# Performance work log

Measured on AMD Instinct MI355X. Metric: run time of the kernel, lower is better.

The kernel has to match this reference:

```python
import jax, jax.numpy as jnp
import numpy as np

C = 128  # num_hidden[-1]; nheads = 1 so dim == C
L, H, W = 16, 96, 96


def conv5(x, w):
    # x: [N, Cin, H, W], w: [1, Cin, 5, 5]; padding=2 -> SAME
    return jax.lax.conv_general_dilated(
        x, w, window_strides=(1, 1), padding=[(2, 2), (2, 2)],
        dimension_numbers=('NCHW', 'OIHW', 'NCHW'))


def setup_inputs() -> dict:
    key = jax.random.key(0)
    ks = jax.random.split(key, 9)
    s = 0.05
    return dict(
        x=jax.random.normal(ks[0], (L, C, H, W), jnp.float32),
        Wq=jax.random.normal(ks[1], (C, C), jnp.float32) * s,
        bq=jax.random.normal(ks[2], (C,), jnp.float32) * s,
        Wk=jax.random.normal(ks[3], (C, C), jnp.float32) * s,
        bk=jax.random.normal(ks[4], (C,), jnp.float32) * s,
        Wv=jax.random.normal(ks[5], (C, C), jnp.float32) * s,
        bv=jax.random.normal(ks[6], (C,), jnp.float32) * s,
        Wa=jax.random.normal(ks[7], (1, 2 * C, 5, 5), jnp.float32) * s,
        ba=jax.random.normal(ks[8], (1,), jnp.float32) * s,
    )


def reference(x, Wq, bq, Wk, bk, Wv, bv, Wa, ba):
    # 1x1 convs == per-pixel linear maps
    Q = jnp.einsum('lchw,dc->ldhw', x, Wq) + bq[None, :, None, None]
    K = jnp.einsum('lchw,dc->ldhw', x, Wk) + bk[None, :, None, None]
    V = jnp.einsum('lchw,dc->ldhw', x, Wv) + bv[None, :, None, None]
    # conv5x5(cat(Qi, Kj)) = conv5x5(Qi; Wa_q) + conv5x5(Kj; Wa_k) + ba
    Aq = conv5(Q, Wa[:, :C])[:, 0]   # [L, H, W]
    Ak = conv5(K, Wa[:, C:])[:, 0]   # [L, H, W]
    S = Aq[:, None] + Ak[None, :] + ba[0]       # [L, L, H, W] score maps H_ij
    A = jax.nn.softmax(S, axis=1)               # softmax over key frame j
    out = jnp.einsum('ijhw,jchw->ichw', A, V)   # weighted sum of V over j
    return out
```

## Files before the change

kernel.cpp:

```cpp
#include <hip/hip_runtime.h>


#define HW    9216
#define HDIM  96
#define WDIM  96
#define CDIM  128
#define WP    28
#define WGS   904

__device__ __forceinline__ void fma4(float4& a, const float4& x, const float4& s) {
    a.x += x.x * s.x; a.y += x.y * s.y; a.z += x.z * s.z; a.w += x.w * s.w;
}
__device__ __forceinline__ void axpy4(float4& o, float w, const float4& v) {
    o.x += w * v.x; o.y += w * v.y; o.z += w * v.z; o.w += w * v.w;
}

__global__ void k_prep(const float* __restrict__ Wk, const float* __restrict__ Wa,
                       const float* __restrict__ Wv,
                       float* __restrict__ weffp, float* __restrict__ wvt) {
    const int b = blockIdx.x;
    if (b < 14) {
        int idx = b * 256 + threadIdx.x;
        if (idx < 128 * WP) {
            int cp = idx / WP, tap = idx % WP;
            float s = 0.f;
            if (tap < 25)
                for (int c = 0; c < 128; ++c)
                    s += Wk[c * 128 + cp] * Wa[(128 + c) * 25 + tap];
            weffp[idx] = s;
        }
    } else {
        int idx = (b - 14) * 256 + threadIdx.x;
        wvt[(idx & 127) * 128 + (idx >> 7)] = Wv[idx];
    }
}

__global__ __launch_bounds__(256, 2) void k_z(const float* __restrict__ x,
                                              const float* __restrict__ weffp,
                                              float* __restrict__ z) {
    __shared__ float wsm[4 * WGS];
    const int tid = threadIdx.x;
    for (int i = tid; i < 4 * WGS; i += 256) {
        int cg = i / WGS, r = i % WGS;
        wsm[i] = (r < 896) ? weffp[cg * 896 + r] : 0.f;
    }
    __syncthreads();

    const int j    = blockIdx.y;
    const int w    = tid >> 6;
    const int lane = tid & 63;
    const int cg   = lane >> 4;
    const int lq   = lane & 15;
    const int px   = blockIdx.x * 256 + w * 64 + lq * 4;

    const float* xb = x + (size_t)(j * CDIM + cg * 32) * HW + px;
    const float* wg = wsm + cg * WGS;

    float4 acc[25];
    #pragma unroll
    for (int t = 0; t < 25; ++t) acc[t] = make_float4(0.f, 0.f, 0.f, 0.f);

    #pragma unroll 2
    for (int c = 0; c < 32; ++c) {
        float4 xv = *(const float4*)(xb + (size_t)c * HW);
        const float* wr = wg + c * WP;
        #pragma unroll
        for (int t = 0; t < 25; ++t) {
            float wv = wr[t];
            acc[t].x = fmaf(wv, xv.x, acc[t].x);
            acc[t].y = fmaf(wv, xv.y, acc[t].y);
            acc[t].z = fmaf(wv, xv.z, acc[t].z);
            acc[t].w = fmaf(wv, xv.w, acc[t].w);
        }
    }
    #pragma unroll
    for (int t = 0; t < 25; ++t) {
        acc[t].x += __shfl_xor(acc[t].x, 16, 64);
        acc[t].y += __shfl_xor(acc[t].y, 16, 64);
        acc[t].z += __shfl_xor(acc[t].z, 16, 64);
        acc[t].w += __shfl_xor(acc[t].w, 16, 64);
        acc[t].x += __shfl_xor(acc[t].x, 32, 64);
        acc[t].y += __shfl_xor(acc[t].y, 32, 64);
        acc[t].z += __shfl_xor(acc[t].z, 32, 64);
        acc[t].w += __shfl_xor(acc[t].w, 32, 64);
    }
    if (cg == 0) {
        float* zb = z + (size_t)j * 25 * HW + px;
        #pragma unroll
        for (int t = 0; t < 25; ++t)
            *(float4*)(zb + (size_t)t * HW) = acc[t];
    }
}

__global__ __launch_bounds__(256) void k_ak(const float* __restrict__ z,
                                            float* __restrict__ ak) {
    const int j  = blockIdx.y;
    const int px = blockIdx.x * 256 + threadIdx.x;
    const int h = px / WDIM, w = px % WDIM;
    const float* zb = z + (size_t)j * 25 * HW + px;
    float s = 0.f;
    #pragma unroll
    for (int kh = 0; kh < 5; ++kh) {
        const bool rok = (unsigned)(h + kh - 2) < (unsigned)HDIM;
        #pragma unroll
        for (int kw = 0; kw < 5; ++kw) {
            const bool ok = rok && ((unsigned)(w + kw - 2) < (unsigned)WDIM);
            const int t = kh * 5 + kw;
            s += ok ? zb[t * HW + (kh - 2) * WDIM + (kw - 2)] : 0.f;
        }
    }
    ak[(size_t)j * HW + px] = s;
}

__global__ __launch_bounds__(192) void k_conv(const float* __restrict__ x,
                                              const float* __restrict__ weffp,
                                              float* __restrict__ part) {
    const int j  = blockIdx.x;
    const int rt = blockIdx.y;
    const int g  = blockIdx.z;
    const int c0 = g * 16;
    __shared__ float tile[36 * 104];
    __shared__ float wsm[16 * WP];
    const int tid = threadIdx.x;
    for (int i = tid; i < 16 * WP; i += 192) wsm[i] = weffp[c0 * WP + i];
    const int cq = tid % 24;
    const int rg = tid / 24;
    const int r0 = rg * 4;
    const int rowbase = rt * 32;

    float4 acc[4];
    acc[0] = acc[1] = acc[2] = acc[3] = make_float4(0.f, 0.f, 0.f, 0.f);

    for (int ch = 0; ch < 16; ++ch) {
        const float* xc = x + (size_t)(j * CDIM + c0 + ch) * HW;
        __syncthreads();
        for (int idx = tid; idx < 36 * 26; idx += 192) {
            int r = idx / 26, q = idx % 26;
            int gr = rowbase - 2 + r;
            int gc = q * 4 - 4;
            float4 v = make_float4(0.f, 0.f, 0.f, 0.f);
            if (gr >= 0 && gr < HDIM && gc >= 0 && gc < WDIM)
                v = *(const float4*)(xc + gr * WDIM + gc);
            *(float4*)(tile + r * 104 + q * 4) = v;
        }
        __syncthreads();
        const float* wc = wsm + ch * WP;
        for (int rr = 0; rr < 8; ++rr) {
            const float* trow = tile + (r0 + rr) * 104 + cq * 4;
            float4 a  = *(const float4*)(trow);
            float4 b  = *(const float4*)(trow + 4);
            float4 c4 = *(const float4*)(trow + 8);
            float win[12] = {a.x, a.y, a.z, a.w, b.x, b.y, b.z, b.w,
                             c4.x, c4.y, c4.z, c4.w};
            #pragma unroll
            for (int orow = 0; orow < 4; ++orow) {
                int kh = rr - orow;
                if (kh < 0 || kh > 4) continue;
                #pragma unroll
                for (int kw = 0; kw < 5; ++kw) {
                    float w = wc[kh * 5 + kw];
                    acc[orow].x += w * win[kw + 2];
                    acc[orow].y += w * win[kw + 3];
                    acc[orow].z += w * win[kw + 4];
                    acc[orow].w += w * win[kw + 5];
                }
            }
        }
    }
    float* pr = part + (size_t)(g * 16 + j) * HW;
    #pragma unroll
    for (int orow = 0; orow < 4; ++orow) {
        int row = rowbase + r0 + orow;
        *(float4*)(pr + row * WDIM + cq * 4) = acc[orow];
    }
}

__global__ void k_combine(const float* __restrict__ part, float* __restrict__ ak) {
    const int j  = blockIdx.y;
    const int px = blockIdx.x * 256 + threadIdx.x;
    float s = 0.f;
    #pragma unroll
    for (int g = 0; g < 8; ++g) s += part[(size_t)(g * 16 + j) * HW + px];
    ak[(size_t)j * HW + px] = s;
}

__global__ __launch_bounds__(256) void k_xbar(const float* __restrict__ x,
                                              const float* __restrict__ ak,
                                              float* __restrict__ xbar) {
    const int b  = blockIdx.x;
    const int cp = b / 9;
    const int px = (b % 9) * 1024 + threadIdx.x * 4;

    float4 av[16];
    #pragma unroll
    for (int j = 0; j < 16; ++j)
        av[j] = *(const float4*)(ak + (size_t)j * HW + px);

    float4 m = av[0];
    #pragma unroll
    for (int j = 1; j < 16; ++j) {
        m.x = fmaxf(m.x, av[j].x); m.y = fmaxf(m.y, av[j].y);
        m.z = fmaxf(m.z, av[j].z); m.w = fmaxf(m.w, av[j].w);
    }
    float4 tot = make_float4(0.f, 0.f, 0.f, 0.f);
    #pragma unroll
    for (int j = 0; j < 16; ++j) {
        av[j].x = __expf(av[j].x - m.x); av[j].y = __expf(av[j].y - m.y);
        av[j].z = __expf(av[j].z - m.z); av[j].w = __expf(av[j].w - m.w);
        tot.x += av[j].x; tot.y += av[j].y; tot.z += av[j].z; tot.w += av[j].w;
    }
    float4 inv = make_float4(1.f / tot.x, 1.f / tot.y, 1.f / tot.z, 1.f / tot.w);

    float4 acc = make_float4(0.f, 0.f, 0.f, 0.f);
    #pragma unroll
    for (int j = 0; j < 16; ++j) {
        float4 xv = *(const float4*)(x + (size_t)(j * CDIM + cp) * HW + px);
        fma4(acc, xv, av[j]);
    }
    acc.x *= inv.x; acc.y *= inv.y; acc.z *= inv.z; acc.w *= inv.w;
    *(float4*)(xbar + (size_t)cp * HW + px) = acc;
}

__global__ __launch_bounds__(256) void k_mat(const float* __restrict__ xbar,
                                             const float* __restrict__ wvt,
                                             const float* __restrict__ bv,
                                             float* __restrict__ out) {
    __shared__ float lx[128 * 16];
    const int b    = blockIdx.x;
    const int half = blockIdx.y;
    const int tile = (b & 7) * 72 + (b >> 3);
    const int px0  = tile * 16;
    const int tid  = threadIdx.x;

    #pragma unroll
    for (int i = 0; i < 2; ++i) {
        int lin = tid + i * 256;
        int cp = lin >> 2, q = lin & 3;
        *(float4*)(lx + cp * 16 + q * 4) =
            *(const float4*)(xbar + (size_t)cp * HW + px0 + q * 4);
    }
    __syncthreads();

    const int q = tid & 3;
    const int c = half * 64 + (tid >> 2);
    float4 o = make_float4(0.f, 0.f, 0.f, 0.f);
    #pragma unroll 4
    for (int cp = 0; cp < 128; ++cp) {
        float4 xv = *(const float4*)(lx + cp * 16 + q * 4);
        axpy4(o, wvt[cp * 128 + c], xv);
    }
    float bb = bv[c];
    o.x += bb; o.y += bb; o.z += bb; o.w += bb;

    for (int i = 0; i < 16; ++i) {
        float* ob = out + (size_t)(i * CDIM + c) * HW + px0 + q * 4;
        *(float4*)(ob) = o;
    }
}

extern "C" void kernel_launch(void* const* d_in, const int* in_sizes, int n_in,
                              void* d_out, int out_size, void* d_ws, size_t ws_size,
                              hipStream_t stream) {
    const float* x  = (const float*)d_in[0];
    const float* Wk = (const float*)d_in[3];
    const float* Wv = (const float*)d_in[5];
    const float* bv = (const float*)d_in[6];
    const float* Wa = (const float*)d_in[7];
    float* out = (float*)d_out;

    char* ws = (char*)d_ws;
    float* weffp = (float*)(ws);
    float* wvt   = (float*)(ws + 16384);

    k_prep<<<78, 256, 0, stream>>>(Wk, Wa, Wv, weffp, wvt);

    const size_t Z_BYTES  = (size_t)16 * 25 * HW * 4;
    const size_t AK_BYTES = (size_t)16 * HW * 4;
    const size_t NEED_BIG = 81920 + Z_BYTES + AK_BYTES;

    if (ws_size >= NEED_BIG) {
        float* z   = (float*)(ws + 81920);
        float* akb = (float*)(ws + 81920 + Z_BYTES);
        float* xb  = (float*)(ws + 81920);
        k_z   <<<dim3(36, 16),  256, 0, stream>>>(x, weffp, z);
        k_ak  <<<dim3(36, 16),  256, 0, stream>>>(z, akb);
        k_xbar<<<1152,          256, 0, stream>>>(x, akb, xb);
        k_mat <<<dim3(576, 2),  256, 0, stream>>>(xb, wvt, bv, out);
    } else {
        float* part = (float*)(ws + 81920);
        float* akb  = (float*)(ws + 81920 + 4718592);
        float* xb   = (float*)(ws + 81920);
        k_conv   <<<dim3(16, 3, 8), 192, 0, stream>>>(x, weffp, part);
        k_combine<<<dim3(36, 16),   256, 0, stream>>>(part, akb);
        k_xbar   <<<1152,           256, 0, stream>>>(x, akb, xb);
        k_mat    <<<dim3(576, 2),   256, 0, stream>>>(xb, wvt, bv, out);
    }
}
```

Before: 88.03 us.

## Split k_z channel groups across waves with LDS reduction, more blocks

Restructures k_z so each wave handles 32 channels for 64 pixels, one pixel per lane, reading the weights from global memory with wave-uniform (scalar) addresses instead of staging them in shared memory. Partial sums from the four waves are combined through shared memory rather than wave shuffles, and the grid grows fourfold to 144x16 blocks. The aim is to cut register pressure (25 floats instead of 25 float4) and the shuffle cost, and to raise occupancy and parallelism. In exchange it adds an LDS write/read pass and loses the float4 vectorised loads.

```diff
diff --git a/kernel.cpp b/kernel.cpp
--- a/kernel.cpp
+++ b/kernel.cpp
@@ -6,7 +6,6 @@
 #define WDIM  96
 #define CDIM  128
 #define WP    28
-#define WGS   904
 
 __device__ __forceinline__ void fma4(float4& a, const float4& x, const float4& s) {
     a.x += x.x * s.x; a.y += x.y * s.y; a.z += x.z * s.z; a.w += x.w * s.w;
@@ -35,60 +34,46 @@
     }
 }
 
-__global__ __launch_bounds__(256, 2) void k_z(const float* __restrict__ x,
-                                              const float* __restrict__ weffp,
-                                              float* __restrict__ z) {
-    __shared__ float wsm[4 * WGS];
-    const int tid = threadIdx.x;
-    for (int i = tid; i < 4 * WGS; i += 256) {
-        int cg = i / WGS, r = i % WGS;
-        wsm[i] = (r < 896) ? weffp[cg * 896 + r] : 0.f;
-    }
-    __syncthreads();
-
+__global__ __launch_bounds__(256) void k_z(const float* __restrict__ x,
+                                           const float* __restrict__ weffp,
+                                           float* __restrict__ z) {
+    __shared__ float red[4 * 25 * 64];
+    const int tid  = threadIdx.x;
+    const int wav  = __builtin_amdgcn_readfirstlane(tid >> 6);
+    const int lane = tid & 63;
     const int j    = blockIdx.y;
-    const int w    = tid >> 6;
-    const int lane = tid & 63;
-    const int cg   = lane >> 4;
-    const int lq   = lane & 15;
-    const int px   = blockIdx.x * 256 + w * 64 + lq * 4;
-
-    const float* xb = x + (size_t)(j * CDIM + cg * 32) * HW + px;
-    const float* wg = wsm + cg * WGS;
-
-    float4 acc[25];
-    #pragma unroll
-    for (int t = 0; t < 25; ++t) acc[t] = make_float4(0.f, 0.f, 0.f, 0.f);
+    const int px0  = blockIdx.x * 64;
+
+    const float* wg = weffp + wav * 32 * WP;
+    const float* xb = x + ((size_t)j * CDIM + wav * 32) * HW + px0 + lane;
+
+    float acc[25];
+    #pragma unroll
+    for (int t = 0; t < 25; ++t) acc[t] = 0.f;
 
     #pragma unroll 2
     for (int c = 0; c < 32; ++c) {
-        float4 xv = *(const float4*)(xb + (size_t)c * HW);
-        const float* wr = wg + c * WP;
-        #pragma unroll
-        for (int t = 0; t < 25; ++t) {
-            float wv = wr[t];
-            acc[t].x = fmaf(wv, xv.x, acc[t].x);
-            acc[t].y = fmaf(wv, xv.y, acc[t].y);
-            acc[t].z = fmaf(wv, xv.z, acc[t].z);
-            acc[t].w = fmaf(wv, xv.w, acc[t].w);
-        }
-    }
-    #pragma unroll
-    for (int t = 0; t < 25; ++t) {
-        acc[t].x += __shfl_xor(acc[t].x, 16, 64);
-        acc[t].y += __shfl_xor(acc[t].y, 16, 64);
-        acc[t].z += __shfl_xor(acc[t].z, 16, 64);
-        acc[t].w += __shfl_xor(acc[t].w, 16, 64);
-        acc[t].x += __shfl_xor(acc[t].x, 32, 64);
-        acc[t].y += __shfl_xor(acc[t].y, 32, 64);
-        acc[t].z += __shfl_xor(acc[t].z, 32, 64);
-        acc[t].w += __shfl_xor(acc[t].w, 32, 64);
-    }
-    if (cg == 0) {
-        float* zb = z + (size_t)j * 25 * HW + px;
+        float xv = xb[(size_t)c * HW];
         #pragma unroll
         for (int t = 0; t < 25; ++t)
-            *(float4*)(zb + (size_t)t * HW) = acc[t];
+            acc[t] = fmaf(wg[c * WP + t], xv, acc[t]);
+    }
+
+    #pragma unroll
+    for (int t = 0; t < 25; ++t)
+        red[(wav * 25 + t) * 64 + lane] = acc[t];
+    __syncthreads();
+
+    float* zb = z + (size_t)j * 25 * HW + px0;
+    #pragma unroll
+    for (int it = 0; it < 7; ++it) {
+        int idx = it * 256 + tid;
+        if (idx < 25 * 64) {
+            int t = idx >> 6, p = idx & 63;
+            float s = red[t * 64 + p] + red[(25 + t) * 64 + p]
+                    + red[(50 + t) * 64 + p] + red[(75 + t) * 64 + p];
+            zb[(size_t)t * HW + p] = s;
+        }
     }
 }
 
@@ -282,7 +267,7 @@
         float* z   = (float*)(ws + 81920);
         float* akb = (float*)(ws + 81920 + Z_BYTES);
         float* xb  = (float*)(ws + 81920);
-        k_z   <<<dim3(36, 16),  256, 0, stream>>>(x, weffp, z);
+        k_z   <<<dim3(144, 16), 256, 0, stream>>>(x, weffp, z);
         k_ak  <<<dim3(36, 16),  256, 0, stream>>>(z, akb);
         k_xbar<<<1152,          256, 0, stream>>>(x, akb, xb);
         k_mat <<<dim3(576, 2),  256, 0, stream>>>(xb, wvt, bv, out);
```

Result: faster. 71.91 us (-18.3%).
